# Kernel tuning notes

Hardware: AMD Instinct MI355X
Metric: run time of the kernel (lower is better)

## Reference

```python
import jax, jax.numpy as jnp
import numpy as np

DIM = 768
NUM_HEADS = 12
SCALE = 1.0 / (DIM ** 0.5)  # NOTE: source scales by 1/sqrt(dim), not 1/sqrt(head_dim)


def setup_inputs() -> dict:
    key = jax.random.key(0)
    k_x, k_qkv, k_ow, k_ob = jax.random.split(key, 4)
    b, n = 8, 1024
    x = jax.random.normal(k_x, (b, n, DIM), dtype=jnp.float32)
    # torch Linear weight is [out, in]; we store jax-style [in, out]
    w_qkv = jax.random.normal(k_qkv, (DIM, 3 * DIM), dtype=jnp.float32) * (DIM ** -0.5)
    w_out = jax.random.normal(k_ow, (DIM, DIM), dtype=jnp.float32) * (DIM ** -0.5)
    b_out = jax.random.normal(k_ob, (DIM,), dtype=jnp.float32) * 0.01
    return {"x": x, "w_qkv": w_qkv, "w_out": w_out, "b_out": b_out}


def reference(x, w_qkv, w_out, b_out):
    b, n, c = x.shape
    h = NUM_HEADS
    hd = c // h
    qkv = (x @ w_qkv).reshape(b, n, 3, h, hd)
    q, k, v = jnp.moveaxis(qkv, 2, 0)          # each [b, n, h, hd]
    q = jnp.swapaxes(q, 1, 2)                  # [b, h, n, hd]
    k = jnp.swapaxes(k, 1, 2)
    v = jnp.swapaxes(v, 1, 2)
    dot = jnp.einsum('bhqd,bhkd->bhqk', q, k) * SCALE
    attn = jax.nn.softmax(dot, axis=-1)        # attn_dropout p=0 -> identity
    out = jnp.einsum('bhqk,bhkd->bhqd', attn, v)
    out = jnp.swapaxes(out, 1, 2).reshape(b, n, c)
    return out @ w_out + b_out                 # proj_dropout p=0 -> identity
```

## Files before the change

### kernel.cpp

```cpp
#include <hip/hip_runtime.h>

#define DEV __device__ __forceinline__

typedef __bf16 bf16x8 __attribute__((ext_vector_type(8)));
typedef float  f32x4  __attribute__((ext_vector_type(4)));
typedef float  f32x16 __attribute__((ext_vector_type(16)));
typedef unsigned int u32x4 __attribute__((ext_vector_type(4)));

static constexpr float SCALE = 0.036084391824351615f;
static constexpr float L2E   = 1.4426950408889634f;

DEV unsigned short f2bf(float f) {
  return __builtin_bit_cast(unsigned short, (__bf16)f);
}
DEV unsigned int pack2(float a, float b) {
  return (unsigned int)f2bf(a) | ((unsigned int)f2bf(b) << 16);
}

#define GLDS16(gp, lp) \
  __builtin_amdgcn_global_load_lds((__attribute__((address_space(1))) void*)(gp), \
                                   (__attribute__((address_space(3))) void*)(lp), 16, 0, 0)

__global__ __launch_bounds__(256) void k_prep(const float* __restrict__ x,
                                              const float* __restrict__ w_qkv,
                                              const float* __restrict__ w_out,
                                              unsigned short* __restrict__ xb,
                                              unsigned short* __restrict__ wqkvT,
                                              unsigned short* __restrict__ woutT) {
  __shared__ float tile[64][65];
  int b = blockIdx.x, t = threadIdx.x;
  if (b < 3072) {
    int i = b * 256 + t;
    const float4* p = (const float4*)x + (size_t)i * 2;
    float4 a = p[0], bb = p[1];
    uint4 r;
    r.x = pack2(a.x, a.y); r.y = pack2(a.z, a.w);
    r.z = pack2(bb.x, bb.y); r.w = pack2(bb.z, bb.w);
    ((uint4*)xb)[i] = r;
    return;
  }
  const float* in;
  unsigned short* out;
  int R, C, bx, by;
  if (b < 3504) {
    int tt = b - 3072; in = w_qkv; out = wqkvT; R = 768; C = 2304;
    bx = tt % 36; by = tt / 36;
  } else {
    int tt = b - 3504; in = w_out; out = woutT; R = 768; C = 768;
    bx = tt % 12; by = tt / 12;
  }
  int c0 = bx * 64, r0 = by * 64;
  int tr = t >> 6, tc = t & 63;
#pragma unroll
  for (int i = 0; i < 64; i += 4)
    tile[i + tr][tc] = in[(size_t)(r0 + i + tr) * C + c0 + tc];
  __syncthreads();
#pragma unroll
  for (int i = 0; i < 64; i += 4)
    out[(size_t)(c0 + i + tr) * R + r0 + tc] = f2bf(tile[tc][i + tr]);
}

template <int MODE>
__global__ __launch_bounds__(256) void k_gemm(const unsigned short* __restrict__ A,
                                              const unsigned short* __restrict__ BT,
                                              void* __restrict__ out0,
                                              unsigned short* __restrict__ Kb,
                                              unsigned short* __restrict__ VTb,
                                              const float* __restrict__ bias) {
  __shared__ __align__(16) char smem[32768];
  char* As = smem;
  char* Bs = smem + 16384;
  const int tid = threadIdx.x;
  const int wave = tid >> 6, lane = tid & 63;
  const int g = lane >> 4, l15 = lane & 15;
  const int wrow = wave >> 1, wcol = wave & 1;

  int id = blockIdx.y * gridDim.x + blockIdx.x;
  int per_xcd = (gridDim.x * gridDim.y) >> 3;
  int id2 = (id & 7) * per_xcd + (id >> 3);
  const int bm = id2 / gridDim.x, bn = id2 % gridDim.x;

  f32x4 acc[4][4] = {};
  const unsigned short* Abase = A + (size_t)bm * 128 * 768;
  const unsigned short* Bbase = BT + (size_t)bn * 128 * 768;

  for (int kt = 0; kt < 12; ++kt) {
    const int k0 = kt * 64;
#pragma unroll
    for (int i = 0; i < 4; ++i) {
      int q = i * 256 + tid;
      int row = q >> 3, c = q & 7;
      int cs = c ^ (row & 7);
      GLDS16(Abase + (size_t)row * 768 + k0 + cs * 8, As + (i * 256 + wave * 64) * 16);
      GLDS16(Bbase + (size_t)row * 768 + k0 + cs * 8, Bs + (i * 256 + wave * 64) * 16);
    }
    __syncthreads();
    __builtin_amdgcn_s_setprio(1);
#pragma unroll
    for (int kk = 0; kk < 2; ++kk) {
      bf16x8 af[4], bfr[4];
#pragma unroll
      for (int mi = 0; mi < 4; ++mi) {
        int r = wrow * 64 + mi * 16 + l15;
        af[mi] = *(const bf16x8*)(As + r * 128 + (((kk * 4 + g) ^ (r & 7)) * 16));
      }
#pragma unroll
      for (int ni = 0; ni < 4; ++ni) {
        int r = wcol * 64 + ni * 16 + l15;
        bfr[ni] = *(const bf16x8*)(Bs + r * 128 + (((kk * 4 + g) ^ (r & 7)) * 16));
      }
#pragma unroll
      for (int mi = 0; mi < 4; ++mi)
#pragma unroll
        for (int ni = 0; ni < 4; ++ni)
          acc[mi][ni] = __builtin_amdgcn_mfma_f32_16x16x32_bf16(af[mi], bfr[ni], acc[mi][ni], 0, 0, 0);
    }
    __builtin_amdgcn_s_setprio(0);
    __syncthreads();
  }

  const int row0 = bm * 128 + wrow * 64;
  const int col0 = bn * 128 + wcol * 64;
#pragma unroll
  for (int mi = 0; mi < 4; ++mi) {
#pragma unroll
    for (int ni = 0; ni < 4; ++ni) {
      int col = col0 + ni * 16 + l15;
      if (MODE == 0) {
        int which = col / 768;
        int hd = col - which * 768;
        int head = hd >> 6, d = hd & 63;
        int rowm0 = row0 + mi * 16 + g * 4;
        int bi = rowm0 >> 10, np = rowm0 & 1023;
        if (which == 0) {
#pragma unroll
          for (int j = 0; j < 4; ++j)
            ((unsigned short*)out0)[((size_t)(bi * 12 + head) * 1024 + np + j) * 64 + d] =
                f2bf(acc[mi][ni][j] * (SCALE * L2E));
        } else if (which == 1) {
#pragma unroll
          for (int j = 0; j < 4; ++j)
            Kb[((size_t)(bi * 12 + head) * 1024 + np + j) * 64 + d] = f2bf(acc[mi][ni][j]);
        } else {
          ushort4 w;
          w.x = f2bf(acc[mi][ni][0]); w.y = f2bf(acc[mi][ni][1]);
          w.z = f2bf(acc[mi][ni][2]); w.w = f2bf(acc[mi][ni][3]);
          *(ushort4*)(VTb + ((size_t)(bi * 12 + head) * 64 + d) * 1024 + np) = w;
        }
      } else {
        float bz = bias[col];
#pragma unroll
        for (int j = 0; j < 4; ++j) {
          int rowm = row0 + mi * 16 + g * 4 + j;
          ((float*)out0)[(size_t)rowm * 768 + col] = acc[mi][ni][j] + bz;
        }
      }
    }
  }
}

__global__ __launch_bounds__(256, 3) void k_attn(const unsigned short* __restrict__ Qb,
                                                 const unsigned short* __restrict__ Kb,
                                                 const unsigned short* __restrict__ VTb,
                                                 unsigned short* __restrict__ Ao) {
  __shared__ __align__(16) char smem[32768];
  const int tid = threadIdx.x, wave = tid >> 6, lane = tid & 63;
  const int hi = lane >> 5, q31 = lane & 31;
  const int bh = blockIdx.x % 96, qt = blockIdx.x / 96;
  const int qbase = qt * 128 + wave * 32;
  const unsigned short* Kp = Kb + (size_t)bh * 65536;
  const unsigned short* Vp = VTb + (size_t)bh * 65536;

  auto STAGE = [&](int buf, int kt) {
#pragma unroll
    for (int i = 0; i < 2; ++i) {
      int c = i * 4 + wave;
      GLDS16(Kp + (size_t)(kt * 64 + lane) * 64 + c * 8,
             smem + buf * 8192 + (i * 256 + wave * 64) * 16);
      GLDS16(Vp + (size_t)lane * 1024 + kt * 64 + c * 8,
             smem + 16384 + buf * 8192 + (i * 256 + wave * 64) * 16);
    }
  };

  bf16x8 aq[4];
#pragma unroll
  for (int dk = 0; dk < 4; ++dk)
    aq[dk] = *(const bf16x8*)(Qb + (size_t)bh * 65536 +
                              (size_t)(qbase + q31) * 64 + dk * 16 + hi * 8);

  bf16x8 vones;
#pragma unroll
  for (int e = 0; e < 8; ++e) vones[e] = (__bf16)1.0f;

  f32x16 o0 = {}, o1 = {};
  f32x16 lacc = {};

  STAGE(0, 0);
  __syncthreads();
  int cur = 0;

  for (int kt = 0; kt < 16; ++kt) {
    if (kt < 15) STAGE(cur ^ 1, kt + 1);
    char* Ks = smem + cur * 8192;
    char* Vs = smem + 16384 + cur * 8192;

    f32x16 st0 = {}, st1 = {};
    __builtin_amdgcn_s_setprio(1);
#pragma unroll
    for (int dk = 0; dk < 4; ++dk) {
      bf16x8 ka0 = *(const bf16x8*)(Ks + (((dk * 2 + hi) * 64 + q31) * 16));
      bf16x8 ka1 = *(const bf16x8*)(Ks + (((dk * 2 + hi) * 64 + 32 + q31) * 16));
      st0 = __builtin_amdgcn_mfma_f32_32x32x16_bf16(ka0, aq[dk], st0, 0, 0, 0);
      st1 = __builtin_amdgcn_mfma_f32_32x32x16_bf16(ka1, aq[dk], st1, 0, 0, 0);
    }
    __builtin_amdgcn_s_setprio(0);

#pragma unroll
    for (int sub = 0; sub < 2; ++sub) {
      const f32x16& st = sub ? st1 : st0;
      float ex[16];
#pragma unroll
      for (int r2 = 0; r2 < 16; ++r2) ex[r2] = __builtin_amdgcn_exp2f(st[r2]);

      unsigned w00 = pack2(ex[0], ex[1]),   w01 = pack2(ex[2], ex[3]);
      unsigned w10 = pack2(ex[4], ex[5]),   w11 = pack2(ex[6], ex[7]);
      unsigned w20 = pack2(ex[8], ex[9]),   w21 = pack2(ex[10], ex[11]);
      unsigned w30 = pack2(ex[12], ex[13]), w31 = pack2(ex[14], ex[15]);

      auto pA = __builtin_amdgcn_permlane32_swap(w00, w10, false, false);
      auto pB = __builtin_amdgcn_permlane32_swap(w01, w11, false, false);
      auto pC = __builtin_amdgcn_permlane32_swap(w20, w30, false, false);
      auto pD = __builtin_amdgcn_permlane32_swap(w21, w31, false, false);

      __builtin_amdgcn_s_setprio(1);
#pragma unroll
      for (int s = 0; s < 2; ++s) {
        u32x4 au;
        if (s == 0) { au[0] = pA[0]; au[1] = pB[0]; au[2] = pA[1]; au[3] = pB[1]; }
        else        { au[0] = pC[0]; au[1] = pD[0]; au[2] = pC[1]; au[3] = pD[1]; }
        bf16x8 pa = __builtin_bit_cast(bf16x8, au);
        int ch = sub * 4 + s * 2 + hi;
        bf16x8 vb0 = *(const bf16x8*)(Vs + (ch * 64 + q31) * 16);
        bf16x8 vb1 = *(const bf16x8*)(Vs + (ch * 64 + 32 + q31) * 16);
        o0   = __builtin_amdgcn_mfma_f32_32x32x16_bf16(pa, vb0, o0, 0, 0, 0);
        o1   = __builtin_amdgcn_mfma_f32_32x32x16_bf16(pa, vb1, o1, 0, 0, 0);
        lacc = __builtin_amdgcn_mfma_f32_32x32x16_bf16(pa, vones, lacc, 0, 0, 0);
      }
      __builtin_amdgcn_s_setprio(0);
    }

    __syncthreads();
    cur ^= 1;
  }

  const int b_idx = bh / 12, h = bh - b_idx * 12;
#pragma unroll
  for (int m = 0; m < 4; ++m) {
#pragma unroll
    for (int j = 0; j < 4; ++j) {
      int reg = m * 4 + j;
      int qr = j + 8 * m + 4 * hi;
      float linv = 1.0f / lacc[reg];
      size_t base = (size_t)(b_idx * 1024 + qbase + qr) * 768 + h * 64 + q31;
      Ao[base]      = f2bf(o0[reg] * linv);
      Ao[base + 32] = f2bf(o1[reg] * linv);
    }
  }
}


extern "C" void kernel_launch(void* const* d_in, const int* in_sizes, int n_in,
                              void* d_out, int out_size, void* d_ws, size_t ws_size,
                              hipStream_t stream) {
  const float* x     = (const float*)d_in[0];
  const float* w_qkv = (const float*)d_in[1];
  const float* w_out = (const float*)d_in[2];
  const float* b_out = (const float*)d_in[3];

  char* ws = (char*)d_ws;
  size_t off = 0;
  auto alloc = [&](size_t bytes) {
    void* p = ws + off;
    off += (bytes + 255) & ~(size_t)255;
    return p;
  };
  unsigned short* xb    = (unsigned short*)alloc(8192ull * 768 * 2);
  unsigned short* wqkvT = (unsigned short*)alloc(2304ull * 768 * 2);
  unsigned short* woutT = (unsigned short*)alloc(768ull * 768 * 2);
  unsigned short* Qb    = (unsigned short*)alloc(96ull * 1024 * 64 * 2);
  unsigned short* Kbf   = (unsigned short*)alloc(96ull * 1024 * 64 * 2);
  unsigned short* VTb   = (unsigned short*)alloc(96ull * 1024 * 64 * 2);
  unsigned short* Aob   = (unsigned short*)alloc(96ull * 1024 * 64 * 2);

  k_prep<<<3648, 256, 0, stream>>>(x, w_qkv, w_out, xb, wqkvT, woutT);
  k_gemm<0><<<dim3(18, 64), 256, 0, stream>>>(xb, wqkvT, Qb, Kbf, VTb, nullptr);
  k_attn<<<768, 256, 0, stream>>>(Qb, Kbf, VTb, Aob);
  k_gemm<1><<<dim3(6, 64), 256, 0, stream>>>(Aob, woutT, d_out, nullptr, nullptr, b_out);
}
```

Measured before the change: 103.9 us.

## Switch attention kernel to 16x16x32 MFMA with 8 waves per block

Rewrites the attention kernel so each wave handles 16 query rows with 16x16x32 bf16 MFMAs instead of 32 rows with 32x32x16. The block grows to 512 threads, and each wave stages one K/V chunk per tile. The softmax probabilities are redistributed with ds_bpermute instead of permlane32_swap. The aim is more waves and fewer registers per wave, for better latency hiding and occupancy. The cost is more LDS reads of K/V per query, because each wave now covers fewer rows, plus extra bpermute shuffle work.

```diff
diff --git a/kernel.cpp b/kernel.cpp
--- a/kernel.cpp
+++ b/kernel.cpp
@@ -4,7 +4,6 @@
 
 typedef __bf16 bf16x8 __attribute__((ext_vector_type(8)));
 typedef float  f32x4  __attribute__((ext_vector_type(4)));
-typedef float  f32x16 __attribute__((ext_vector_type(16)));
 typedef unsigned int u32x4 __attribute__((ext_vector_type(4)));
 
 static constexpr float SCALE = 0.036084391824351615f;
@@ -159,41 +158,41 @@
   }
 }
 
-__global__ __launch_bounds__(256, 3) void k_attn(const unsigned short* __restrict__ Qb,
+__global__ __launch_bounds__(512, 6) void k_attn(const unsigned short* __restrict__ Qb,
                                                  const unsigned short* __restrict__ Kb,
                                                  const unsigned short* __restrict__ VTb,
                                                  unsigned short* __restrict__ Ao) {
   __shared__ __align__(16) char smem[32768];
   const int tid = threadIdx.x, wave = tid >> 6, lane = tid & 63;
-  const int hi = lane >> 5, q31 = lane & 31;
+  const int g = (lane >> 4) & 3, l15 = lane & 15;
+  const int ghi = g >> 1;
   const int bh = blockIdx.x % 96, qt = blockIdx.x / 96;
-  const int qbase = qt * 128 + wave * 32;
+  const int qw = qt * 128 + wave * 16;
   const unsigned short* Kp = Kb + (size_t)bh * 65536;
   const unsigned short* Vp = VTb + (size_t)bh * 65536;
 
   auto STAGE = [&](int buf, int kt) {
-#pragma unroll
-    for (int i = 0; i < 2; ++i) {
-      int c = i * 4 + wave;
-      GLDS16(Kp + (size_t)(kt * 64 + lane) * 64 + c * 8,
-             smem + buf * 8192 + (i * 256 + wave * 64) * 16);
-      GLDS16(Vp + (size_t)lane * 1024 + kt * 64 + c * 8,
-             smem + 16384 + buf * 8192 + (i * 256 + wave * 64) * 16);
-    }
+    GLDS16(Kp + (size_t)(kt * 64 + lane) * 64 + wave * 8,
+           smem + buf * 8192 + wave * 1024);
+    GLDS16(Vp + (size_t)lane * 1024 + kt * 64 + wave * 8,
+           smem + 16384 + buf * 8192 + wave * 1024);
   };
 
-  bf16x8 aq[4];
-#pragma unroll
-  for (int dk = 0; dk < 4; ++dk)
+  bf16x8 aq[2];
+#pragma unroll
+  for (int dk = 0; dk < 2; ++dk)
     aq[dk] = *(const bf16x8*)(Qb + (size_t)bh * 65536 +
-                              (size_t)(qbase + q31) * 64 + dk * 16 + hi * 8);
+                              (size_t)(qw + l15) * 64 + dk * 32 + g * 8);
 
   bf16x8 vones;
 #pragma unroll
   for (int e = 0; e < 8; ++e) vones[e] = (__bf16)1.0f;
 
-  f32x16 o0 = {}, o1 = {};
-  f32x16 lacc = {};
+  f32x4 o[4] = {};
+  f32x4 lacc = {};
+
+  const int addr0 = (l15 + 16 * (2 * (g & 1) + 0)) * 4;
+  const int addr1 = (l15 + 16 * (2 * (g & 1) + 1)) * 4;
 
   STAGE(0, 0);
   __syncthreads();
@@ -204,48 +203,51 @@
     char* Ks = smem + cur * 8192;
     char* Vs = smem + 16384 + cur * 8192;
 
-    f32x16 st0 = {}, st1 = {};
+    f32x4 st[4] = {};
     __builtin_amdgcn_s_setprio(1);
 #pragma unroll
-    for (int dk = 0; dk < 4; ++dk) {
-      bf16x8 ka0 = *(const bf16x8*)(Ks + (((dk * 2 + hi) * 64 + q31) * 16));
-      bf16x8 ka1 = *(const bf16x8*)(Ks + (((dk * 2 + hi) * 64 + 32 + q31) * 16));
-      st0 = __builtin_amdgcn_mfma_f32_32x32x16_bf16(ka0, aq[dk], st0, 0, 0, 0);
-      st1 = __builtin_amdgcn_mfma_f32_32x32x16_bf16(ka1, aq[dk], st1, 0, 0, 0);
-    }
+    for (int dk = 0; dk < 2; ++dk)
+#pragma unroll
+      for (int kf = 0; kf < 4; ++kf) {
+        bf16x8 ka = *(const bf16x8*)(Ks + ((dk * 4 + g) * 64 + kf * 16 + l15) * 16);
+        st[kf] = __builtin_amdgcn_mfma_f32_16x16x32_bf16(ka, aq[dk], st[kf], 0, 0, 0);
+      }
     __builtin_amdgcn_s_setprio(0);
 
-#pragma unroll
-    for (int sub = 0; sub < 2; ++sub) {
-      const f32x16& st = sub ? st1 : st0;
-      float ex[16];
-#pragma unroll
-      for (int r2 = 0; r2 < 16; ++r2) ex[r2] = __builtin_amdgcn_exp2f(st[r2]);
-
-      unsigned w00 = pack2(ex[0], ex[1]),   w01 = pack2(ex[2], ex[3]);
-      unsigned w10 = pack2(ex[4], ex[5]),   w11 = pack2(ex[6], ex[7]);
-      unsigned w20 = pack2(ex[8], ex[9]),   w21 = pack2(ex[10], ex[11]);
-      unsigned w30 = pack2(ex[12], ex[13]), w31 = pack2(ex[14], ex[15]);
-
-      auto pA = __builtin_amdgcn_permlane32_swap(w00, w10, false, false);
-      auto pB = __builtin_amdgcn_permlane32_swap(w01, w11, false, false);
-      auto pC = __builtin_amdgcn_permlane32_swap(w20, w30, false, false);
-      auto pD = __builtin_amdgcn_permlane32_swap(w21, w31, false, false);
+    unsigned own[4][2];
+#pragma unroll
+    for (int kf = 0; kf < 4; ++kf)
+#pragma unroll
+      for (int p = 0; p < 2; ++p)
+        own[kf][p] = pack2(__builtin_amdgcn_exp2f(st[kf][2 * p]),
+                           __builtin_amdgcn_exp2f(st[kf][2 * p + 1]));
+
+#pragma unroll
+    for (int ks = 0; ks < 2; ++ks) {
+      u32x4 au;
+      {
+        int c0 = __builtin_amdgcn_ds_bpermute(addr0, (int)own[2 * ks][0]);
+        int c1 = __builtin_amdgcn_ds_bpermute(addr0, (int)own[2 * ks + 1][0]);
+        au[0] = (unsigned)(ghi ? c1 : c0);
+        c0 = __builtin_amdgcn_ds_bpermute(addr0, (int)own[2 * ks][1]);
+        c1 = __builtin_amdgcn_ds_bpermute(addr0, (int)own[2 * ks + 1][1]);
+        au[1] = (unsigned)(ghi ? c1 : c0);
+        c0 = __builtin_amdgcn_ds_bpermute(addr1, (int)own[2 * ks][0]);
+        c1 = __builtin_amdgcn_ds_bpermute(addr1, (int)own[2 * ks + 1][0]);
+        au[2] = (unsigned)(ghi ? c1 : c0);
+        c0 = __builtin_amdgcn_ds_bpermute(addr1, (int)own[2 * ks][1]);
+        c1 = __builtin_amdgcn_ds_bpermute(addr1, (int)own[2 * ks + 1][1]);
+        au[3] = (unsigned)(ghi ? c1 : c0);
+      }
+      bf16x8 pa = __builtin_bit_cast(bf16x8, au);
 
       __builtin_amdgcn_s_setprio(1);
 #pragma unroll
-      for (int s = 0; s < 2; ++s) {
-        u32x4 au;
-        if (s == 0) { au[0] = pA[0]; au[1] = pB[0]; au[2] = pA[1]; au[3] = pB[1]; }
-        else        { au[0] = pC[0]; au[1] = pD[0]; au[2] = pC[1]; au[3] = pD[1]; }
-        bf16x8 pa = __builtin_bit_cast(bf16x8, au);
-        int ch = sub * 4 + s * 2 + hi;
-        bf16x8 vb0 = *(const bf16x8*)(Vs + (ch * 64 + q31) * 16);
-        bf16x8 vb1 = *(const bf16x8*)(Vs + (ch * 64 + 32 + q31) * 16);
-        o0   = __builtin_amdgcn_mfma_f32_32x32x16_bf16(pa, vb0, o0, 0, 0, 0);
-        o1   = __builtin_amdgcn_mfma_f32_32x32x16_bf16(pa, vb1, o1, 0, 0, 0);
-        lacc = __builtin_amdgcn_mfma_f32_32x32x16_bf16(pa, vones, lacc, 0, 0, 0);
-      }
+      for (int df = 0; df < 4; ++df) {
+        bf16x8 vb = *(const bf16x8*)(Vs + ((ks * 4 + g) * 64 + df * 16 + l15) * 16);
+        o[df] = __builtin_amdgcn_mfma_f32_16x16x32_bf16(pa, vb, o[df], 0, 0, 0);
+      }
+      lacc = __builtin_amdgcn_mfma_f32_16x16x32_bf16(pa, vones, lacc, 0, 0, 0);
       __builtin_amdgcn_s_setprio(0);
     }
 
@@ -255,16 +257,12 @@
 
   const int b_idx = bh / 12, h = bh - b_idx * 12;
 #pragma unroll
-  for (int m = 0; m < 4; ++m) {
-#pragma unroll
-    for (int j = 0; j < 4; ++j) {
-      int reg = m * 4 + j;
-      int qr = j + 8 * m + 4 * hi;
-      float linv = 1.0f / lacc[reg];
-      size_t base = (size_t)(b_idx * 1024 + qbase + qr) * 768 + h * 64 + q31;
-      Ao[base]      = f2bf(o0[reg] * linv);
-      Ao[base + 32] = f2bf(o1[reg] * linv);
-    }
+  for (int j = 0; j < 4; ++j) {
+    float linv = 1.0f / lacc[j];
+    size_t base = (size_t)(b_idx * 1024 + qw + 4 * g + j) * 768 + h * 64 + l15;
+#pragma unroll
+    for (int df = 0; df < 4; ++df)
+      Ao[base + df * 16] = f2bf(o[df][j] * linv);
   }
 }
 
@@ -294,6 +292,6 @@
 
   k_prep<<<3648, 256, 0, stream>>>(x, w_qkv, w_out, xb, wqkvT, woutT);
   k_gemm<0><<<dim3(18, 64), 256, 0, stream>>>(xb, wqkvT, Qb, Kbf, VTb, nullptr);
-  k_attn<<<768, 256, 0, stream>>>(Qb, Kbf, VTb, Aob);
+  k_attn<<<768, 512, 0, stream>>>(Qb, Kbf, VTb, Aob);
   k_gemm<1><<<dim3(6, 64), 256, 0, stream>>>(Aob, woutT, d_out, nullptr, nullptr, b_out);
 }
```

New measurement: 107.5 us. 3.4% more time.
